# Optimization experiments

Measured on AMD Instinct MI355X. Metric: run time of the kernel, lower is better.

The kernel has to match this reference:

```python
import jax, jax.numpy as jnp
import numpy as np

GRID = 25
NUM_NODE = GRID * GRID  # 625, hard-coded by the original module

def _neighbor_flat_indices():
    # Replicates the torch index construction exactly, incl. boundary shifts.
    offsets = np.array([[-1,-1],[-1,0],[-1,1],[0,-1],[0,0],[0,1],[1,-1],[1,0],[1,1]])
    idx = np.arange(NUM_NODE)
    rows = idx // GRID
    cols = idx % GRID
    nr = rows[:, None] + offsets[:, 0]   # [625, 9]
    nc = cols[:, None] + offsets[:, 1]
    nr = nr.reshape(GRID, GRID, 9)
    nr[0, :, :] += 1                     # reflect top boundary
    nr[-1, :, :] -= 1                    # reflect bottom boundary
    nr = nr.reshape(NUM_NODE, 9)
    nc = nc.reshape(GRID, GRID, 9)
    nc[:, 0, :] += 1                     # reflect left boundary
    nc[:, -1, :] -= 1                    # reflect right boundary
    nc = nc.reshape(NUM_NODE, 9)
    return jnp.asarray(nr * GRID + nc)   # [625, 9] flat node indices

NEIGH = _neighbor_flat_indices()

def setup_inputs() -> dict:
    key = jax.random.key(0)
    k1, k2, k3, k4, k5 = jax.random.split(key, 5)
    B = 512
    x = jax.random.normal(k1, (B, NUM_NODE, 66), dtype=jnp.float32)
    # nn.Linear(66, 64): weight [64, 66], bias [64]
    W_fc = jax.random.normal(k2, (64, 66), dtype=jnp.float32) * (1.0 / np.sqrt(66))
    b_fc = jax.random.normal(k3, (64,), dtype=jnp.float32) * 0.01
    # nn.Linear(128, 1): weight [1, 128], bias [1]
    W_at = jax.random.normal(k4, (1, 128), dtype=jnp.float32) * (1.0 / np.sqrt(128))
    b_at = jax.random.normal(k5, (1,), dtype=jnp.float32) * 0.01
    return {"x": x, "W_fc": W_fc, "b_fc": b_fc, "W_at": W_at, "b_at": b_at}

def reference(x, W_fc, b_fc, W_at, b_at):
    # h = fc(x): [B, 625, 64]
    h = jnp.einsum('bnf,df->bnd', x, W_fc) + b_fc
    # Gather fixed 9-neighbor features: [B, 625, 9, 64]
    x2 = h[:, NEIGH, :]
    # Center feature broadcast to the 9 neighbor slots: [B, 625, 9, 64]
    x1 = jnp.broadcast_to(h[:, :, None, :], x2.shape)
    z = jnp.concatenate([x1, x2], axis=-1)                  # [B, 625, 9, 128]
    s = jnp.einsum('bnkf,of->bnko', z, W_at) + b_at          # [B, 625, 9, 1]
    s = jax.nn.leaky_relu(s, negative_slope=0.01)[..., 0]    # [B, 625, 9]
    # exp(s) / sum(exp(s)) over the 9 neighbors == softmax(s)
    attn_weight = jax.nn.softmax(s, axis=-1)                 # [B, 625, 9]
    # Original: sum_k h[:, :, None, :] * w[..., None] over k
    # = h * sum_k w  (h does not depend on k); avoids a [B,625,9,64] temp.
    attn_vector = h * jnp.sum(attn_weight, axis=-1, keepdims=True)  # [B, 625, 64]
    return (attn_vector, attn_weight)
```

## Files before the change

kernel.cpp:

```cpp
#include <hip/hip_runtime.h>

#define BATCH 512
#define GRID_N 25
#define NODES 625
#define BN (BATCH * NODES)
#define NTILES (BN / 16)
#define F 66
#define D 64
#define WPB 4
#define TPW 2
#define NBLOCKS (NTILES / (WPB * TPW))

typedef short bf16x8 __attribute__((ext_vector_type(8)));
typedef float f32x4  __attribute__((ext_vector_type(4)));

__device__ __forceinline__ short f2bf(float f) {
    union { float f; unsigned u; } c; c.f = f;
    unsigned r = c.u + 0x7fffu + ((c.u >> 16) & 1u);
    return (short)(r >> 16);
}

__global__ __launch_bounds__(256, 3) void fc_mfma(
    const float* __restrict__ x, const float* __restrict__ Wfc,
    const float* __restrict__ bfc, const float* __restrict__ Wat,
    float* __restrict__ hout, float* __restrict__ u, float* __restrict__ v)
{
    const int tid  = threadIdx.x;
    const int lane = tid & 63;
    const int wid  = tid >> 6;
    const int l15  = lane & 15;
    const int quad = lane >> 4;
    const int gw   = blockIdx.x * WPB + wid;
    const int tile0 = gw * TPW;

    __shared__ float smem[WPB * 256 * 4];
    float* tbuf = smem + wid * 1024;

    float2 xb[TPW][9];
#pragma unroll
    for (int t = 0; t < TPW; ++t) {
        const float2* rp = (const float2*)x + (size_t)(tile0 + t) * 528 + l15 * 33;
#pragma unroll
        for (int j2 = 0; j2 < 4; ++j2) xb[t][j2]     = rp[quad * 4 + j2];
#pragma unroll
        for (int j2 = 0; j2 < 4; ++j2) xb[t][4 + j2] = rp[16 + quad * 4 + j2];
        if (quad == 0) xb[t][8] = rp[32];
    }

    bf16x8 bfrag[4][3];
#pragma unroll
    for (int t = 0; t < 4; ++t) {
        const float2* wr = (const float2*)Wfc + (t * 16 + l15) * 33;
#pragma unroll
        for (int c = 0; c < 2; ++c) {
            bf16x8 fr;
#pragma unroll
            for (int j2 = 0; j2 < 4; ++j2) {
                const float2 p = wr[c * 16 + quad * 4 + j2];
                fr[j2 * 2]     = f2bf(p.x);
                fr[j2 * 2 + 1] = f2bf(p.y);
            }
            bfrag[t][c] = fr;
        }
        bf16x8 z = {0, 0, 0, 0, 0, 0, 0, 0};
        if (quad == 0) {
            const float2 p = wr[32];
            z[0] = f2bf(p.x); z[1] = f2bf(p.y);
        }
        bfrag[t][2] = z;
    }
    float bft[4], wa1[4], wa2[4];
#pragma unroll
    for (int t = 0; t < 4; ++t) {
        bft[t] = bfc[t * 16 + l15];
        wa1[t] = Wat[t * 16 + l15];
        wa2[t] = Wat[64 + t * 16 + l15];
    }

#pragma unroll
    for (int t = 0; t < TPW; ++t) {
        const int bn0 = (tile0 + t) * 16;

        bf16x8 afrag[3];
#pragma unroll
        for (int c = 0; c < 2; ++c) {
            bf16x8 fr;
#pragma unroll
            for (int j2 = 0; j2 < 4; ++j2) {
                const float2 p = xb[t][c * 4 + j2];
                fr[j2 * 2]     = f2bf(p.x);
                fr[j2 * 2 + 1] = f2bf(p.y);
            }
            afrag[c] = fr;
        }
        {
            bf16x8 z = {0, 0, 0, 0, 0, 0, 0, 0};
            if (quad == 0) { z[0] = f2bf(xb[t][8].x); z[1] = f2bf(xb[t][8].y); }
            afrag[2] = z;
        }

        f32x4 acc[4] = {{0,0,0,0},{0,0,0,0},{0,0,0,0},{0,0,0,0}};
#pragma unroll
        for (int nt = 0; nt < 4; ++nt)
#pragma unroll
            for (int c = 0; c < 3; ++c)
                acc[nt] = __builtin_amdgcn_mfma_f32_16x16x32_bf16(afrag[c], bfrag[nt][c], acc[nt], 0, 0, 0);

        float pu[4] = {0, 0, 0, 0}, pv[4] = {0, 0, 0, 0};
#pragma unroll
        for (int nt = 0; nt < 4; ++nt) {
#pragma unroll
            for (int r = 0; r < 4; ++r) {
                const float h = acc[nt][r] + bft[nt];
                tbuf[(quad * 4 + r) * 64 + nt * 16 + l15] = h;
                pu[r] = fmaf(h, wa1[nt], pu[r]);
                pv[r] = fmaf(h, wa2[nt], pv[r]);
            }
        }
#pragma unroll
        for (int off = 8; off > 0; off >>= 1) {
#pragma unroll
            for (int r = 0; r < 4; ++r) {
                pu[r] += __shfl_xor(pu[r], off, 64);
                pv[r] += __shfl_xor(pv[r], off, 64);
            }
        }
        if (l15 == 0) {
#pragma unroll
            for (int r = 0; r < 4; ++r) {
                u[bn0 + quad * 4 + r] = pu[r];
                v[bn0 + quad * 4 + r] = pv[r];
            }
        }
        float4* dst = (float4*)(hout + (size_t)bn0 * D);
        const float4* src = (const float4*)tbuf;
#pragma unroll
        for (int i = 0; i < 4; ++i)
            dst[i * 64 + lane] = src[i * 64 + lane];
    }
}

__global__ __launch_bounds__(256) void attn_kernel(
    const float* __restrict__ u, const float* __restrict__ v,
    const float* __restrict__ bat, float* __restrict__ wout)
{
    __shared__ float sw[256 * 9];
    const int tid  = threadIdx.x;
    const int lane = tid & 63;
    const int wid  = tid >> 6;
    const int bn   = blockIdx.x * 256 + tid;

    const int b   = bn / NODES;
    const int n   = bn - b * NODES;
    const int row = n / GRID_N;
    const int col = n - row * GRID_N;
    const int r0 = row + (row == 0) - (row == GRID_N - 1);
    const int c0 = col + (col == 0) - (col == GRID_N - 1);

    const float* vb = v + b * NODES;
    const float u0 = u[bn] + bat[0];

    float s[9];
#pragma unroll
    for (int k = 0; k < 9; ++k) {
        const int nr = r0 + (k / 3) - 1;
        const int nc = c0 + (k % 3) - 1;
        const float t = u0 + vb[nr * GRID_N + nc];
        s[k] = (t >= 0.0f) ? t : 0.01f * t;
    }
    float m = s[0];
#pragma unroll
    for (int k = 1; k < 9; ++k) m = fmaxf(m, s[k]);
    float sum = 0.0f;
#pragma unroll
    for (int k = 0; k < 9; ++k) { s[k] = __expf(s[k] - m); sum += s[k]; }
    const float inv = 1.0f / sum;

    float* ws = sw + wid * 576;
#pragma unroll
    for (int k = 0; k < 9; ++k) ws[lane * 9 + k] = s[k] * inv;

    float4* dst = (float4*)(wout + (size_t)(blockIdx.x * 256 + wid * 64) * 9);
    const float4* src = (const float4*)ws;
    dst[lane]      = src[lane];
    dst[64 + lane] = src[64 + lane];
    if (lane < 16) dst[128 + lane] = src[128 + lane];
}

extern "C" void kernel_launch(void* const* d_in, const int* in_sizes, int n_in,
                              void* d_out, int out_size, void* d_ws, size_t ws_size,
                              hipStream_t stream)
{
    const float* x   = (const float*)d_in[0];
    const float* Wfc = (const float*)d_in[1];
    const float* bfc = (const float*)d_in[2];
    const float* Wat = (const float*)d_in[3];
    const float* bat = (const float*)d_in[4];

    float* hout = (float*)d_out;
    float* wout = (float*)d_out + (size_t)BN * D;
    float* u = (float*)d_ws;
    float* v = u + BN;

    fc_mfma<<<NBLOCKS, 256, 0, stream>>>(x, Wfc, bfc, Wat, hout, u, v);
    attn_kernel<<<BN / 256, 256, 0, stream>>>(u, v, bat, wout);
}
```

Baseline: 176.4 us.

## Stage converted weight fragments in LDS and process one tile per wave

The bf16 weight fragments are now converted cooperatively once per block into shared memory, where previously every wave held them in registers. Each wave now handles one 16-row tile instead of two, with launch bounds raised to six blocks per CU to increase occupancy. The h output is written directly from the accumulators instead of being staged through LDS for float4 stores, and u/v are stored as float4. In exchange, the kernel launches twice as many blocks, each redoing the weight conversion, adds a block barrier, and the h stores become strided 4-byte writes that may coalesce less well.

```diff
diff --git a/kernel.cpp b/kernel.cpp
--- a/kernel.cpp
+++ b/kernel.cpp
@@ -7,9 +7,6 @@
 #define NTILES (BN / 16)
 #define F 66
 #define D 64
-#define WPB 4
-#define TPW 2
-#define NBLOCKS (NTILES / (WPB * TPW))
 
 typedef short bf16x8 __attribute__((ext_vector_type(8)));
 typedef float f32x4  __attribute__((ext_vector_type(4)));
@@ -20,7 +17,7 @@
     return (short)(r >> 16);
 }
 
-__global__ __launch_bounds__(256, 3) void fc_mfma(
+__global__ __launch_bounds__(256, 6) void fc_mfma(
     const float* __restrict__ x, const float* __restrict__ Wfc,
     const float* __restrict__ bfc, const float* __restrict__ Wat,
     float* __restrict__ hout, float* __restrict__ u, float* __restrict__ v)
@@ -30,45 +27,42 @@
     const int wid  = tid >> 6;
     const int l15  = lane & 15;
     const int quad = lane >> 4;
-    const int gw   = blockIdx.x * WPB + wid;
-    const int tile0 = gw * TPW;
 
-    __shared__ float smem[WPB * 256 * 4];
-    float* tbuf = smem + wid * 1024;
+    __shared__ bf16x8 Bl[12][64];
 
-    float2 xb[TPW][9];
 #pragma unroll
-    for (int t = 0; t < TPW; ++t) {
-        const float2* rp = (const float2*)x + (size_t)(tile0 + t) * 528 + l15 * 33;
-#pragma unroll
-        for (int j2 = 0; j2 < 4; ++j2) xb[t][j2]     = rp[quad * 4 + j2];
-#pragma unroll
-        for (int j2 = 0; j2 < 4; ++j2) xb[t][4 + j2] = rp[16 + quad * 4 + j2];
-        if (quad == 0) xb[t][8] = rp[32];
-    }
-
-    bf16x8 bfrag[4][3];
-#pragma unroll
-    for (int t = 0; t < 4; ++t) {
-        const float2* wr = (const float2*)Wfc + (t * 16 + l15) * 33;
-#pragma unroll
-        for (int c = 0; c < 2; ++c) {
-            bf16x8 fr;
+    for (int e = tid; e < 768; e += 256) {
+        const int ln = e & 63;
+        const int tc = e >> 6;
+        const int t  = tc / 3, c = tc - 3 * t;
+        const int L  = ln & 15, Q = ln >> 4;
+        const float2* wr = (const float2*)Wfc + (t * 16 + L) * 33;
+        bf16x8 fr = {0, 0, 0, 0, 0, 0, 0, 0};
+        if (c < 2) {
 #pragma unroll
             for (int j2 = 0; j2 < 4; ++j2) {
-                const float2 p = wr[c * 16 + quad * 4 + j2];
+                const float2 p = wr[c * 16 + Q * 4 + j2];
                 fr[j2 * 2]     = f2bf(p.x);
                 fr[j2 * 2 + 1] = f2bf(p.y);
             }
-            bfrag[t][c] = fr;
+        } else if (Q == 0) {
+            const float2 p = wr[32];
+            fr[0] = f2bf(p.x); fr[1] = f2bf(p.y);
         }
-        bf16x8 z = {0, 0, 0, 0, 0, 0, 0, 0};
-        if (quad == 0) {
-            const float2 p = wr[32];
-            z[0] = f2bf(p.x); z[1] = f2bf(p.y);
-        }
-        bfrag[t][2] = z;
+        Bl[tc][ln] = fr;
     }
+
+    const int tile = blockIdx.x * 4 + wid;
+    const int bn0  = tile * 16;
+    const float2* rp = (const float2*)x + (size_t)tile * 528 + l15 * 33;
+    float2 xb[9];
+#pragma unroll
+    for (int j2 = 0; j2 < 4; ++j2) {
+        xb[j2]     = rp[quad * 4 + j2];
+        xb[4 + j2] = rp[16 + quad * 4 + j2];
+    }
+    xb[8] = rp[32];
+
     float bft[4], wa1[4], wa2[4];
 #pragma unroll
     for (int t = 0; t < 4; ++t) {
@@ -77,66 +71,62 @@
         wa2[t] = Wat[64 + t * 16 + l15];
     }
 
+    bf16x8 afrag[3];
 #pragma unroll
-    for (int t = 0; t < TPW; ++t) {
-        const int bn0 = (tile0 + t) * 16;
+    for (int c = 0; c < 2; ++c) {
+        bf16x8 fr;
+#pragma unroll
+        for (int j2 = 0; j2 < 4; ++j2) {
+            const float2 p = xb[c * 4 + j2];
+            fr[j2 * 2]     = f2bf(p.x);
+            fr[j2 * 2 + 1] = f2bf(p.y);
+        }
+        afrag[c] = fr;
+    }
+    {
+        bf16x8 z = {0, 0, 0, 0, 0, 0, 0, 0};
+        if (quad == 0) { z[0] = f2bf(xb[8].x); z[1] = f2bf(xb[8].y); }
+        afrag[2] = z;
+    }
 
-        bf16x8 afrag[3];
+    __syncthreads();
+
+    f32x4 acc[4] = {{0,0,0,0},{0,0,0,0},{0,0,0,0},{0,0,0,0}};
 #pragma unroll
-        for (int c = 0; c < 2; ++c) {
-            bf16x8 fr;
+    for (int c = 0; c < 3; ++c) {
+        const bf16x8 b0 = Bl[c][lane];
+        const bf16x8 b1 = Bl[3 + c][lane];
+        const bf16x8 b2 = Bl[6 + c][lane];
+        const bf16x8 b3 = Bl[9 + c][lane];
+        acc[0] = __builtin_amdgcn_mfma_f32_16x16x32_bf16(afrag[c], b0, acc[0], 0, 0, 0);
+        acc[1] = __builtin_amdgcn_mfma_f32_16x16x32_bf16(afrag[c], b1, acc[1], 0, 0, 0);
+        acc[2] = __builtin_amdgcn_mfma_f32_16x16x32_bf16(afrag[c], b2, acc[2], 0, 0, 0);
+        acc[3] = __builtin_amdgcn_mfma_f32_16x16x32_bf16(afrag[c], b3, acc[3], 0, 0, 0);
+        __builtin_amdgcn_sched_barrier(0);
+    }
+
+    float pu[4] = {0, 0, 0, 0}, pv[4] = {0, 0, 0, 0};
 #pragma unroll
-            for (int j2 = 0; j2 < 4; ++j2) {
-                const float2 p = xb[t][c * 4 + j2];
-                fr[j2 * 2]     = f2bf(p.x);
-                fr[j2 * 2 + 1] = f2bf(p.y);
-            }
-            afrag[c] = fr;
+    for (int nt = 0; nt < 4; ++nt) {
+#pragma unroll
+        for (int r = 0; r < 4; ++r) {
+            const float h = acc[nt][r] + bft[nt];
+            hout[(size_t)(bn0 + quad * 4 + r) * D + nt * 16 + l15] = h;
+            pu[r] = fmaf(h, wa1[nt], pu[r]);
+            pv[r] = fmaf(h, wa2[nt], pv[r]);
         }
-        {
-            bf16x8 z = {0, 0, 0, 0, 0, 0, 0, 0};
-            if (quad == 0) { z[0] = f2bf(xb[t][8].x); z[1] = f2bf(xb[t][8].y); }
-            afrag[2] = z;
+    }
+#pragma unroll
+    for (int off = 8; off > 0; off >>= 1) {
+#pragma unroll
+        for (int r = 0; r < 4; ++r) {
+            pu[r] += __shfl_xor(pu[r], off, 64);
+            pv[r] += __shfl_xor(pv[r], off, 64);
         }
-
-        f32x4 acc[4] = {{0,0,0,0},{0,0,0,0},{0,0,0,0},{0,0,0,0}};
-#pragma unroll
-        for (int nt = 0; nt < 4; ++nt)
-#pragma unroll
-            for (int c = 0; c < 3; ++c)
-                acc[nt] = __builtin_amdgcn_mfma_f32_16x16x32_bf16(afrag[c], bfrag[nt][c], acc[nt], 0, 0, 0);
-
-        float pu[4] = {0, 0, 0, 0}, pv[4] = {0, 0, 0, 0};
-#pragma unroll
-        for (int nt = 0; nt < 4; ++nt) {
-#pragma unroll
-            for (int r = 0; r < 4; ++r) {
-                const float h = acc[nt][r] + bft[nt];
-                tbuf[(quad * 4 + r) * 64 + nt * 16 + l15] = h;
-                pu[r] = fmaf(h, wa1[nt], pu[r]);
-                pv[r] = fmaf(h, wa2[nt], pv[r]);
-            }
-        }
-#pragma unroll
-        for (int off = 8; off > 0; off >>= 1) {
-#pragma unroll
-            for (int r = 0; r < 4; ++r) {
-                pu[r] += __shfl_xor(pu[r], off, 64);
-                pv[r] += __shfl_xor(pv[r], off, 64);
-            }
-        }
-        if (l15 == 0) {
-#pragma unroll
-            for (int r = 0; r < 4; ++r) {
-                u[bn0 + quad * 4 + r] = pu[r];
-                v[bn0 + quad * 4 + r] = pv[r];
-            }
-        }
-        float4* dst = (float4*)(hout + (size_t)bn0 * D);
-        const float4* src = (const float4*)tbuf;
-#pragma unroll
-        for (int i = 0; i < 4; ++i)
-            dst[i * 64 + lane] = src[i * 64 + lane];
+    }
+    if (l15 == 0) {
+        *(float4*)(u + bn0 + quad * 4) = make_float4(pu[0], pu[1], pu[2], pu[3]);
+        *(float4*)(v + bn0 + quad * 4) = make_float4(pv[0], pv[1], pv[2], pv[3]);
     }
 }
 
@@ -202,6 +192,6 @@
     float* u = (float*)d_ws;
     float* v = u + BN;
 
-    fc_mfma<<<NBLOCKS, 256, 0, stream>>>(x, Wfc, bfc, Wat, hout, u, v);
+    fc_mfma<<<NTILES / 4, 256, 0, stream>>>(x, Wfc, bfc, Wat, hout, u, v);
     attn_kernel<<<BN / 256, 256, 0, stream>>>(u, v, bat, wout);
 }
```

Result: faster. 170.8 us (-3.2%).
